# Optimization experiments

Measured on AMD Instinct MI355X. Metric: run time of the kernel, lower is better.

## Reference

```python
import jax, jax.numpy as jnp
import numpy as np

V = 4096   # input_dim (one-hot / vocab size)
H = 256    # hidden_dim
O = 512    # output_dim
B = 64     # batch
T = 512    # sequence length


def setup_inputs() -> dict:
    key = jax.random.key(0)
    ks = jax.random.split(key, 7)
    s = 1.0 / np.sqrt(H)  # PyTorch nn.RNN / nn.Linear init range
    x = jax.random.randint(ks[0], (B, T), 0, V)
    W_ih = jax.random.uniform(ks[1], (H, V), minval=-s, maxval=s, dtype=jnp.float32)
    W_hh = jax.random.uniform(ks[2], (H, H), minval=-s, maxval=s, dtype=jnp.float32)
    b_ih = jax.random.uniform(ks[3], (H,), minval=-s, maxval=s, dtype=jnp.float32)
    b_hh = jax.random.uniform(ks[4], (H,), minval=-s, maxval=s, dtype=jnp.float32)
    W_fc = jax.random.uniform(ks[5], (O, H), minval=-s, maxval=s, dtype=jnp.float32)
    b_fc = jax.random.uniform(ks[6], (O,), minval=-s, maxval=s, dtype=jnp.float32)
    return {"x": x, "W_ih": W_ih, "W_hh": W_hh, "b_ih": b_ih, "b_hh": b_hh,
            "W_fc": W_fc, "b_fc": b_fc}


def reference(x, W_ih, W_hh, b_ih, b_hh, W_fc, b_fc):
    # one_hot(x, V).float() @ W_ih.T is algebraically a row-gather of W_ih.T
    x_proj = jnp.take(W_ih.T, x, axis=0) + b_ih  # [B, T, H]

    def step(h, xt):
        h = jnp.tanh(xt + h @ W_hh.T + b_hh)  # vanilla tanh RNN cell
        return h, h

    h0 = jnp.zeros((x.shape[0], W_hh.shape[0]), dtype=x_proj.dtype)
    _, hs = jax.lax.scan(step, h0, jnp.swapaxes(x_proj, 0, 1))  # [T, B, H]
    hs = jnp.swapaxes(hs, 0, 1)  # [B, T, H]
    return hs @ W_fc.T + b_fc  # [B, T, O]
```

## Files before the change

kernel.cpp:

```cpp
#include <hip/hip_runtime.h>

#define V 4096
#define H 256
#define O 512
#define B 64
#define T 512

typedef __attribute__((ext_vector_type(8))) short bf16x8;
typedef __attribute__((ext_vector_type(4))) float f32x4;
typedef __attribute__((ext_vector_type(2))) float f32x2;

__device__ __forceinline__ unsigned short f2bf(float f) {
    unsigned int u = __float_as_uint(f);
    u += 0x7fffu + ((u >> 16) & 1u);
    return (unsigned short)(u >> 16);
}
__device__ __forceinline__ float bf2f(unsigned short s) {
    return __uint_as_float(((unsigned int)s) << 16);
}

__device__ __forceinline__ float dpp_xor1(float v) {
    int i = __float_as_int(v);
    return __int_as_float(__builtin_amdgcn_update_dpp(i, i, 0xB1, 0xf, 0xf, true));
}
__device__ __forceinline__ float dpp_xor2(float v) {
    int i = __float_as_int(v);
    return __int_as_float(__builtin_amdgcn_update_dpp(i, i, 0x4E, 0xf, 0xf, true));
}
__device__ __forceinline__ float dpp_ror8(float v) {
    int i = __float_as_int(v);
    return __int_as_float(__builtin_amdgcn_update_dpp(i, i, 0x128, 0xf, 0xf, true));
}

__global__ __launch_bounds__(256) void k_transpose(const float* __restrict__ Wih,
                                                   float* __restrict__ WihT) {
    __shared__ float tile[64][65];
    const int bi = blockIdx.x & 3;
    const int bv = blockIdx.x >> 2;
    const int tx = threadIdx.x & 63, ty = threadIdx.x >> 6;
#pragma unroll
    for (int s = 0; s < 16; ++s) {
        int r = ty + 4 * s;
        tile[r][tx] = Wih[(size_t)(bi * 64 + r) * V + bv * 64 + tx];
    }
    __syncthreads();
#pragma unroll
    for (int s = 0; s < 16; ++s) {
        int r = ty + 4 * s;
        WihT[(size_t)(bv * 64 + r) * H + bi * 64 + tx] = tile[tx][r];
    }
}

__global__ __launch_bounds__(256) void k_prep(const float* __restrict__ Wfc,
                                              unsigned short* __restrict__ hi,
                                              unsigned short* __restrict__ lo) {
    int i = blockIdx.x * 256 + threadIdx.x;
    float w = Wfc[i];
    unsigned short h = f2bf(w);
    hi[i] = h;
    lo[i] = f2bf(w - bf2f(h));
}

#define CH16 20

__global__ __launch_bounds__(512, 2) void k_rnn(
    const int* __restrict__ x, const float* __restrict__ WihT,
    const float* __restrict__ Whh, const float* __restrict__ b_ih,
    const float* __restrict__ b_hh,
    unsigned short* __restrict__ hs_hi) {
    __shared__ float hsm[2][16 * CH16];
    __shared__ int xs[T];
    const int b = blockIdx.x;
    const int tid = threadIdx.x;
    const int g = tid >> 4;
    const int c = tid & 15;
    const int cr = c & 7;
    const int row = 8 * g + cr;
    const int k0 = 16 * c;

    f32x2 w2[8][8];
#pragma unroll
    for (int r = 0; r < 8; ++r) {
        const f32x2* wr = (const f32x2*)(Whh + (size_t)(8 * g + r) * H + k0);
#pragma unroll
        for (int q = 0; q < 8; ++q) w2[r][q] = wr[q];
    }
#pragma unroll
    for (int r = 0; r < 8; ++r)
#pragma unroll
        for (int q = 0; q < 8; ++q)
            asm volatile("" : "+v"(w2[r][q]));

    xs[tid] = x[b * T + tid];
    if (tid < 16 * CH16) hsm[0][tid] = 0.0f;
    const float bias = b_ih[row] + b_hh[row];
    __syncthreads();

    unsigned short* ph = hs_hi + (size_t)b * T * H + row;

    float xp_cur = WihT[(size_t)xs[0] * H + row];
    unsigned short h_prev = 0;

    for (int t = 0; t < T; ++t) {
        if (t > 0 && c < 8)
            __builtin_nontemporal_store(h_prev, &ph[(size_t)(t - 1) * H]);
        int tn = (t + 1 < T) ? t + 1 : t;
        float xp_next = WihT[(size_t)xs[tn] * H + row];

        const f32x4* hv = (const f32x4*)&hsm[t & 1][c * CH16];
        f32x4 q0 = hv[0], q1 = hv[1], q2 = hv[2], q3 = hv[3];
        f32x2 h2[8] = {{q0[0], q0[1]}, {q0[2], q0[3]}, {q1[0], q1[1]}, {q1[2], q1[3]},
                       {q2[0], q2[1]}, {q2[2], q2[3]}, {q3[0], q3[1]}, {q3[2], q3[3]}};
        f32x2 a0 = {0,0}, a1 = {0,0}, a2 = {0,0}, a3 = {0,0};
        f32x2 a4 = {0,0}, a5 = {0,0}, a6 = {0,0}, a7 = {0,0};
#pragma unroll
        for (int q = 0; q < 8; ++q) {
            a0 += h2[q] * w2[0][q];
            a1 += h2[q] * w2[1][q];
            a2 += h2[q] * w2[2][q];
            a3 += h2[q] * w2[3][q];
            a4 += h2[q] * w2[4][q];
            a5 += h2[q] * w2[5][q];
            a6 += h2[q] * w2[6][q];
            a7 += h2[q] * w2[7][q];
        }
        float s0 = a0[0] + a0[1], s1 = a1[0] + a1[1];
        float s2 = a2[0] + a2[1], s3 = a3[0] + a3[1];
        float s4 = a4[0] + a4[1], s5 = a5[0] + a5[1];
        float s6 = a6[0] + a6[1], s7 = a7[0] + a7[1];
        s0 += dpp_xor1(s0); s1 += dpp_xor1(s1); s2 += dpp_xor1(s2); s3 += dpp_xor1(s3);
        s4 += dpp_xor1(s4); s5 += dpp_xor1(s5); s6 += dpp_xor1(s6); s7 += dpp_xor1(s7);
        const bool b0 = c & 1, b1 = c & 2, b2 = c & 4;
        float u0 = b0 ? s1 : s0;
        float u1 = b0 ? s3 : s2;
        float u2 = b0 ? s5 : s4;
        float u3 = b0 ? s7 : s6;
        u0 += dpp_xor2(u0); u1 += dpp_xor2(u1); u2 += dpp_xor2(u2); u3 += dpp_xor2(u3);
        float v0 = b1 ? u1 : u0;
        float v1 = b1 ? u3 : u2;
        v0 += __int_as_float(__builtin_amdgcn_ds_swizzle(__float_as_int(v0), 0x101F));
        v1 += __int_as_float(__builtin_amdgcn_ds_swizzle(__float_as_int(v1), 0x101F));
        float own = b2 ? v1 : v0;
        own += dpp_ror8(own);

        float pre = own + xp_cur + bias;
        float e = __expf(2.0f * pre);
        float hval = 1.0f - 2.0f * __builtin_amdgcn_rcpf(e + 1.0f);

        if (c < 8)
            hsm[(t + 1) & 1][(row >> 4) * CH16 + (row & 15)] = hval;
        h_prev = f2bf(hval);
        xp_cur = xp_next;

#pragma unroll
        for (int r = 0; r < 8; ++r)
#pragma unroll
            for (int q = 0; q < 8; ++q)
                asm volatile("" : "+v"(w2[r][q]));

        asm volatile("s_waitcnt lgkmcnt(0)" ::: "memory");
        __builtin_amdgcn_s_barrier();
        asm volatile("" ::: "memory");
    }
    if (c < 8) ph[(size_t)(T - 1) * H] = h_prev;
}

__global__ __launch_bounds__(256, 2) void k_fc(
    const unsigned short* __restrict__ hs_hi,
    const unsigned short* __restrict__ wfc_hi, const unsigned short* __restrict__ wfc_lo,
    const float* __restrict__ b_fc, float* __restrict__ out) {
    __shared__ short sA[128 * 64], sBh[128 * 64], sBl[128 * 64];
    const int tid = threadIdx.x;
    const int bm = blockIdx.x >> 2, bn = blockIdx.x & 3;
    const int m0 = bm * 128, n0 = bn * 128;
    const int w = tid >> 6, lane = tid & 63;
    const int wm = w >> 1, wn = w & 1;
    const int l16 = lane & 15, g = lane >> 4;

    f32x4 acc[4][4];
#pragma unroll
    for (int a = 0; a < 4; ++a)
#pragma unroll
        for (int cc = 0; cc < 4; ++cc)
#pragma unroll
            for (int qq = 0; qq < 4; ++qq) acc[a][cc][qq] = 0.0f;

    for (int kt = 0; kt < 4; ++kt) {
        const int k0 = kt * 64;
#pragma unroll
        for (int s = 0; s < 4; ++s) {
            int cidx = tid + 256 * s;
            int r = cidx >> 3, slot = cidx & 7;
            int dst = r * 64 + ((slot ^ (r & 7)) << 3);
            size_t ga = (size_t)(m0 + r) * 256 + k0 + slot * 8;
            *(bf16x8*)&sA[dst] = *(const bf16x8*)&hs_hi[ga];
            size_t gb = (size_t)(n0 + r) * 256 + k0 + slot * 8;
            *(bf16x8*)&sBh[dst] = *(const bf16x8*)&wfc_hi[gb];
            *(bf16x8*)&sBl[dst] = *(const bf16x8*)&wfc_lo[gb];
        }
        __syncthreads();
#pragma unroll
        for (int kc = 0; kc < 2; ++kc) {
            bf16x8 ah[4], bh[4], bl[4];
            const int slot = kc * 4 + g;
#pragma unroll
            for (int mi = 0; mi < 4; ++mi) {
                int r = wm * 64 + mi * 16 + l16;
                int off = r * 64 + ((slot ^ (r & 7)) << 3);
                ah[mi] = *(const bf16x8*)&sA[off];
            }
#pragma unroll
            for (int ni = 0; ni < 4; ++ni) {
                int r = wn * 64 + ni * 16 + l16;
                int off = r * 64 + ((slot ^ (r & 7)) << 3);
                bh[ni] = *(const bf16x8*)&sBh[off];
                bl[ni] = *(const bf16x8*)&sBl[off];
            }
#pragma unroll
            for (int mi = 0; mi < 4; ++mi)
#pragma unroll
                for (int ni = 0; ni < 4; ++ni) {
                    acc[mi][ni] = __builtin_amdgcn_mfma_f32_16x16x32_bf16(
                        ah[mi], bh[ni], acc[mi][ni], 0, 0, 0);
                    acc[mi][ni] = __builtin_amdgcn_mfma_f32_16x16x32_bf16(
                        ah[mi], bl[ni], acc[mi][ni], 0, 0, 0);
                }
        }
        __syncthreads();
    }
#pragma unroll
    for (int ni = 0; ni < 4; ++ni) {
        int n = n0 + wn * 64 + ni * 16 + l16;
        float bfc = b_fc[n];
#pragma unroll
        for (int mi = 0; mi < 4; ++mi) {
#pragma unroll
            for (int qq = 0; qq < 4; ++qq) {
                int m = m0 + wm * 64 + mi * 16 + g * 4 + qq;
                out[(size_t)m * O + n] = acc[mi][ni][qq] + bfc;
            }
        }
    }
}

extern "C" void kernel_launch(void* const* d_in, const int* in_sizes, int n_in,
                              void* d_out, int out_size, void* d_ws, size_t ws_size,
                              hipStream_t stream) {
    (void)in_sizes; (void)n_in; (void)out_size; (void)ws_size;
    const int*   x    = (const int*)d_in[0];
    const float* Wih  = (const float*)d_in[1];
    const float* Whh  = (const float*)d_in[2];
    const float* bih  = (const float*)d_in[3];
    const float* bhh  = (const float*)d_in[4];
    const float* Wfc  = (const float*)d_in[5];
    const float* bfc  = (const float*)d_in[6];
    float* out = (float*)d_out;

    char* ws = (char*)d_ws;
    float*          WihT = (float*)ws;
    unsigned short* wfch = (unsigned short*)(ws + 4194304);
    unsigned short* wfcl = (unsigned short*)(ws + 4194304 + 262144);
    unsigned short* hsh  = (unsigned short*)(ws + 4718592);

    k_transpose<<<256, 256, 0, stream>>>(Wih, WihT);
    k_prep<<<512, 256, 0, stream>>>(Wfc, wfch, wfcl);
    k_rnn<<<64, 512, 0, stream>>>(x, WihT, Whh, bih, bhh, hsh);
    k_fc<<<1024, 256, 0, stream>>>(hsh, wfch, wfcl, bfc, out);
}
```

Before: 345.6 us.

## Replace ds_swizzle with DPP reduction and move hs store after barrier

Swaps the ds_swizzle butterfly step in the recurrent reduction for two DPP row-rotates, so the per-step reduction stays in VALU and no longer uses LDS. Drops the shared xs token buffer in favour of per-step global loads of x two steps ahead. Moves the bf16 hidden-state store after the barrier and removes the asm register pins on the W_hh fragments. The removed pins and the extra global load on the serial path risk register spills or added latency.

```diff
diff --git a/kernel.cpp b/kernel.cpp
--- a/kernel.cpp
+++ b/kernel.cpp
@@ -26,6 +26,10 @@
 __device__ __forceinline__ float dpp_xor2(float v) {
     int i = __float_as_int(v);
     return __int_as_float(__builtin_amdgcn_update_dpp(i, i, 0x4E, 0xf, 0xf, true));
+}
+__device__ __forceinline__ float dpp_ror4(float v) {
+    int i = __float_as_int(v);
+    return __int_as_float(__builtin_amdgcn_update_dpp(i, i, 0x124, 0xf, 0xf, true));
 }
 __device__ __forceinline__ float dpp_ror8(float v) {
     int i = __float_as_int(v);
@@ -69,13 +73,11 @@
     const float* __restrict__ b_hh,
     unsigned short* __restrict__ hs_hi) {
     __shared__ float hsm[2][16 * CH16];
-    __shared__ int xs[T];
     const int b = blockIdx.x;
     const int tid = threadIdx.x;
+    const int c = tid & 15;
     const int g = tid >> 4;
-    const int c = tid & 15;
-    const int cr = c & 7;
-    const int row = 8 * g + cr;
+    const int row = 8 * g + (c & 7);
     const int k0 = 16 * c;
 
     f32x2 w2[8][8];
@@ -85,27 +87,18 @@
 #pragma unroll
         for (int q = 0; q < 8; ++q) w2[r][q] = wr[q];
     }
-#pragma unroll
-    for (int r = 0; r < 8; ++r)
-#pragma unroll
-        for (int q = 0; q < 8; ++q)
-            asm volatile("" : "+v"(w2[r][q]));
-
-    xs[tid] = x[b * T + tid];
+
     if (tid < 16 * CH16) hsm[0][tid] = 0.0f;
     const float bias = b_ih[row] + b_hh[row];
     __syncthreads();
 
-    unsigned short* ph = hs_hi + (size_t)b * T * H + row;
-
-    float xp_cur = WihT[(size_t)xs[0] * H + row];
-    unsigned short h_prev = 0;
+    const int bT = b * T;
+    int x0 = x[bT];
+    int xt1 = x[bT + 1];
+    float xp_cur = WihT[(size_t)x0 * H + row];
 
     for (int t = 0; t < T; ++t) {
-        if (t > 0 && c < 8)
-            __builtin_nontemporal_store(h_prev, &ph[(size_t)(t - 1) * H]);
-        int tn = (t + 1 < T) ? t + 1 : t;
-        float xp_next = WihT[(size_t)xs[tn] * H + row];
+        float xp_next = WihT[(size_t)xt1 * H + row];
 
         const f32x4* hv = (const f32x4*)&hsm[t & 1][c * CH16];
         f32x4 q0 = hv[0], q1 = hv[1], q2 = hv[2], q3 = hv[3];
@@ -138,10 +131,9 @@
         u0 += dpp_xor2(u0); u1 += dpp_xor2(u1); u2 += dpp_xor2(u2); u3 += dpp_xor2(u3);
         float v0 = b1 ? u1 : u0;
         float v1 = b1 ? u3 : u2;
-        v0 += __int_as_float(__builtin_amdgcn_ds_swizzle(__float_as_int(v0), 0x101F));
-        v1 += __int_as_float(__builtin_amdgcn_ds_swizzle(__float_as_int(v1), 0x101F));
+        v0 += dpp_ror4(v0); v1 += dpp_ror4(v1);
+        v0 += dpp_ror8(v0); v1 += dpp_ror8(v1);
         float own = b2 ? v1 : v0;
-        own += dpp_ror8(own);
 
         float pre = own + xp_cur + bias;
         float e = __expf(2.0f * pre);
@@ -149,20 +141,17 @@
 
         if (c < 8)
             hsm[(t + 1) & 1][(row >> 4) * CH16 + (row & 15)] = hval;
-        h_prev = f2bf(hval);
-        xp_cur = xp_next;
-
-#pragma unroll
-        for (int r = 0; r < 8; ++r)
-#pragma unroll
-            for (int q = 0; q < 8; ++q)
-                asm volatile("" : "+v"(w2[r][q]));
 
         asm volatile("s_waitcnt lgkmcnt(0)" ::: "memory");
         __builtin_amdgcn_s_barrier();
-        asm volatile("" ::: "memory");
-    }
-    if (c < 8) ph[(size_t)(T - 1) * H] = h_prev;
+
+        if (c < 8)
+            __builtin_nontemporal_store(
+                f2bf(hval), &hs_hi[(size_t)(bT + t) * H + row]);
+        xp_cur = xp_next;
+        int tnn = (t + 2 < T) ? t + 2 : T - 1;
+        xt1 = x[bT + tnn];
+    }
 }
 
 __global__ __launch_bounds__(256, 2) void k_fc(
```

Measured after the change: 361.2 us. 1.05x slower.
